# Kernel optimization log

Hardware: AMD Instinct MI355X
Metric: run time of the kernel (lower is better)

Reference implementation:

```python
import jax, jax.numpy as jnp
import numpy as np

N, E = 131072, 64
REL_SIZES = {0: (262144, 1), 1: (524288, 2), 2: (393216, 3)}  # idx_len, arity


def _mish(x):
    return x * jnp.tanh(jax.nn.softplus(x))


def _mlp(x, rw, rb, ow, ob):
    # torch MLP: output(input + mish(residual(input)))
    return (x + _mish(x @ rw + rb)) @ ow + ob


def setup_inputs() -> dict:
    key = jax.random.key(0)
    ks = jax.random.split(key, 16)

    def lin(k, fi, fo):
        k1, k2 = jax.random.split(k)
        lim = 1.0 / np.sqrt(fi)
        w = jax.random.uniform(k1, (fi, fo), jnp.float32, -lim, lim)
        b = jax.random.uniform(k2, (fo,), jnp.float32, -lim, lim)
        return w, b

    inp = {"obj_emb": jax.random.normal(ks[0], (N, E), jnp.float32)}
    for r in range(3):
        L, _ = REL_SIZES[r]
        inp[f"rel{r}_idx"] = jax.random.randint(ks[1 + r], (L,), 0, N, jnp.int64)
    for r in range(3):
        _, a = REL_SIZES[r]
        d = a * E
        w, b = lin(ks[4 + 2 * r], d, d)
        inp[f"r{r}_res_w"], inp[f"r{r}_res_b"] = w, b
        w, b = lin(ks[5 + 2 * r], d, d)
        inp[f"r{r}_out_w"], inp[f"r{r}_out_b"] = w, b
    w, b = lin(ks[10], 2 * E, 2 * E)
    inp["upd_res_w"], inp["upd_res_b"] = w, b
    w, b = lin(ks[11], 2 * E, E)
    inp["upd_out_w"], inp["upd_out_b"] = w, b
    return inp


def _forward(obj_emb, idxs, rel_params, upd_params):
    n, e = obj_emb.shape
    outs = []
    for (idx, a), (rw, rb, ow, ob) in zip(idxs, rel_params):
        g = obj_emb[idx].reshape(-1, a * e)          # gather -> [T, a*E]
        outs.append((idx, _mlp(g, rw, rb, ow, ob).reshape(-1, e)))
    # First scatter_reduce_('amax', include_self=False): positions written by
    # relation 0 ignore the initial 0; all other positions keep/compete with 0.
    written0 = jnp.zeros((n,), bool).at[idxs[0][0]].set(True)
    m = jnp.broadcast_to(jnp.where(written0[:, None], -jnp.inf, 0.0).astype(obj_emb.dtype), (n, e))
    for idx, out in outs:
        m = m.at[idx].max(out)
    m = jax.lax.stop_gradient(m)
    s = jnp.full((n, e), 1e-16, obj_emb.dtype)
    for idx, out in outs:
        s = s.at[idx].add(jnp.exp(12.0 * (out - m[idx])))
    max_msg = jnp.log(s) / 12.0 + m
    return _mlp(jnp.concatenate([max_msg, obj_emb], axis=1), *upd_params)


def reference(obj_emb, rel0_idx, rel1_idx, rel2_idx,
              r0_res_w, r0_res_b, r0_out_w, r0_out_b,
              r1_res_w, r1_res_b, r1_out_w, r1_out_b,
              r2_res_w, r2_res_b, r2_out_w, r2_out_b,
              upd_res_w, upd_res_b, upd_out_w, upd_out_b):
    idxs = [(rel0_idx, 1), (rel1_idx, 2), (rel2_idx, 3)]
    rel_params = [
        (r0_res_w, r0_res_b, r0_out_w, r0_out_b),
        (r1_res_w, r1_res_b, r1_out_w, r1_out_b),
        (r2_res_w, r2_res_b, r2_out_w, r2_out_b),
    ]
    return _forward(obj_emb, idxs, rel_params,
                    (upd_res_w, upd_res_b, upd_out_w, upd_out_b))
```

## Files before the change

### kernel.cpp

```cpp
#include <hip/hip_runtime.h>
#include <stdint.h>

typedef unsigned short u16;
typedef __bf16 bf16x8 __attribute__((ext_vector_type(8)));
typedef float floatx4 __attribute__((ext_vector_type(4)));

#define N_OBJ    131072
#define L0R      262144
#define L1R      524288
#define L2R      393216
#define TOTI     (L0R + L1R + L2R)


__device__ __forceinline__ float bf2f(u16 u) {
  union { uint32_t i; float f; } v; v.i = ((uint32_t)u) << 16; return v.f;
}
__device__ __forceinline__ u16 f2bf(float f) {
  union { float f; uint32_t i; } v; v.f = f;
  uint32_t r = (v.i + 0x7FFFu + ((v.i >> 16) & 1u)) >> 16;
  return (u16)r;
}
__device__ __forceinline__ uint4 pack8(const float* sp) {
  float4 f0 = *(const float4*)(sp);
  float4 f1 = *(const float4*)(sp + 4);
  uint4 v;
  v.x = (uint32_t)f2bf(f0.x) | ((uint32_t)f2bf(f0.y) << 16);
  v.y = (uint32_t)f2bf(f0.z) | ((uint32_t)f2bf(f0.w) << 16);
  v.z = (uint32_t)f2bf(f1.x) | ((uint32_t)f2bf(f1.y) << 16);
  v.w = (uint32_t)f2bf(f1.z) | ((uint32_t)f2bf(f1.w) << 16);
  return v;
}
__device__ __forceinline__ float mish_f(float x) {
  float t = __expf(fminf(x, 30.f));
  float u = 1.f + t; u = u * u;
  return x * (u - 1.f) / (u + 1.f);
}

__global__ __launch_bounds__(256) void ebf_kernel(
    const float* __restrict__ src, u16* __restrict__ dst)
{
  size_t g = (size_t)blockIdx.x * 256 + threadIdx.x;
  *(uint4*)(dst + g * 8) = pack8(src + g * 8);
}

__global__ __launch_bounds__(256) void norm_kernel(
    const int* __restrict__ r0, const int* __restrict__ r1,
    const int* __restrict__ r2, int* __restrict__ n, int* __restrict__ cnt,
    unsigned char* __restrict__ flag)
{
  int g = blockIdx.x * 256 + (int)threadIdx.x;
  const int* src; int off;
  if (g < L0R)              { src = r0; off = g; }
  else if (g < L0R + L1R)   { src = r1; off = g - L0R; }
  else                      { src = r2; off = g - L0R - L1R; }
  int lane = (int)threadIdx.x & 63;
  int probe = src[2 * lane + 1];
  bool i64 = (__ballot(probe == 0) == ~0ull);
  int v = i64 ? src[2 * off] : src[off];
  n[g] = v;
  if (g < L0R) flag[v] = 1;
  if (cnt) atomicAdd(&cnt[v], 1);
}

__global__ __launch_bounds__(256) void prep_kernel(
    const float* w0, const float* w1, const float* w2, const float* w3,
    const float* w4, const float* w5, const float* w6, const float* w7,
    u16* __restrict__ wt)
{
  int b = blockIdx.x;
  const float* srcs[8] = {w0, w1, w2, w3, w4, w5, w6, w7};
  const int fi[8]   = {64, 64, 128, 128, 192, 192, 128, 128};
  const int fo[8]   = {64, 64, 128, 128, 192, 192, 128, 64};
  const int boff[9] = {0, 16, 32, 96, 160, 304, 448, 512, 544};
  const int woff[8] = {0, 4096, 8192, 24576, 40960, 77824, 114688, 131072};
  int m = 0;
  #pragma unroll
  for (int j = 0; j < 8; ++j) if (b >= boff[j + 1]) m = j + 1;
  int e = (b - boff[m]) * 256 + (int)threadIdx.x;
  int k = e / fo[m];
  int n = e - k * fo[m];
  wt[woff[m] + n * fi[m] + k] = f2bf(srcs[m][e]);
}

__global__ __launch_bounds__(256) void scan_a(
    const int* __restrict__ count, int* __restrict__ thrpre,
    int* __restrict__ blocksum)
{
  int tid = (int)threadIdx.x, b = blockIdx.x;
  int o = b * 1024 + tid * 4;
  int t = count[o] + count[o + 1] + count[o + 2] + count[o + 3];
  __shared__ int sd[256];
  sd[tid] = t; __syncthreads();
  for (int off = 1; off < 256; off <<= 1) {
    int v = (tid >= off) ? sd[tid - off] : 0;
    __syncthreads();
    sd[tid] += v;
    __syncthreads();
  }
  thrpre[b * 256 + tid] = sd[tid] - t;
  if (tid == 255) blocksum[b] = sd[tid];
}
__global__ __launch_bounds__(128) void scan_b(int* __restrict__ blocksum)
{
  int tid = (int)threadIdx.x;
  int t = blocksum[tid];
  __shared__ int sd[128];
  sd[tid] = t; __syncthreads();
  for (int off = 1; off < 128; off <<= 1) {
    int v = (tid >= off) ? sd[tid - off] : 0;
    __syncthreads();
    sd[tid] += v;
    __syncthreads();
  }
  blocksum[tid] = sd[tid] - t;
}
__global__ __launch_bounds__(256) void scan_c(
    const int* __restrict__ count, const int* __restrict__ thrpre,
    const int* __restrict__ blocksum, int* __restrict__ offsets,
    int* __restrict__ cursor)
{
  int tid = (int)threadIdx.x, b = blockIdx.x;
  int o = b * 1024 + tid * 4;
  int base = blocksum[b] + thrpre[b * 256 + tid];
  #pragma unroll
  for (int j = 0; j < 4; ++j) {
    offsets[o + j] = base;
    cursor[o + j] = base;
    base += count[o + j];
  }
}

template<int D, int DOUT, int EBF>
__device__ __forceinline__ void mlp_body(
    char* smem, const float* __restrict__ srcF, const u16* __restrict__ srcB,
    const int* __restrict__ idx, int bidx,
    const u16* __restrict__ rwt, const float* __restrict__ rb,
    const u16* __restrict__ owt, const float* __restrict__ ob,
    u16* __restrict__ msg, int* __restrict__ cursor)
{
  constexpr int A = D / 64;
  constexpr int PITCH = D + 8;
  constexpr int KI = D / 32;
  constexpr int CT1 = D / 64;
  constexpr int CT2 = DOUT / 64;
  u16*   g_lds  = (u16*)smem;
  float* b1_lds = (float*)(smem + 64 * PITCH * 2);
  float* b2_lds = b1_lds + D;
  int*   i_lds  = (int*)(b2_lds + DOUT);
  int*   p_lds  = i_lds + 64 * A;

  const int tid = threadIdx.x;
  const int wave = tid >> 6;
  const int lane = tid & 63;
  const int q = lane >> 4;
  const int i = lane & 15;
  const int t0 = bidx * 64;

  for (int c = tid; c < D; c += 256) b1_lds[c] = rb[c];
  for (int c = tid; c < DOUT; c += 256) b2_lds[c] = ob[c];
  for (int c = tid; c < 64 * A; c += 256) {
    int obj = idx[t0 * A + c];
    i_lds[c] = obj;
    p_lds[c] = atomicAdd(&cursor[obj], 1);
  }

  for (int c = tid; c < 64 * A * 8; c += 256) {
    int e = c >> 3, p = c & 7;
    int r = e / A, sl = e - r * A;
    int obj = idx[(t0 + r) * A + sl];
    uint4 val = EBF ? *(const uint4*)(srcB + (size_t)obj * 64 + p * 8)
                    : pack8(srcF + (size_t)obj * 64 + p * 8);
    *(uint4*)(&g_lds[r * PITCH + sl * 64 + p * 8]) = val;
  }
  __syncthreads();

  bf16x8 af[KI];

  bf16x8 b1[CT1][KI];
  #pragma unroll
  for (int j = 0; j < CT1; ++j)
    #pragma unroll
    for (int k = 0; k < KI; ++k)
      b1[j][k] = *(const bf16x8*)(rwt +
          (size_t)((wave * CT1 + j) * 16 + i) * D + k * 32 + q * 8);

  floatx4 acc1[4][CT1];
  #pragma unroll
  for (int rt = 0; rt < 4; ++rt)
    #pragma unroll
    for (int j = 0; j < CT1; ++j) acc1[rt][j] = (floatx4)0.f;

  #pragma unroll
  for (int rt = 0; rt < 4; ++rt) {
    #pragma unroll
    for (int k = 0; k < KI; ++k)
      af[k] = *(const bf16x8*)(&g_lds[(rt * 16 + i) * PITCH + k * 32 + q * 8]);
    #pragma unroll
    for (int j = 0; j < CT1; ++j)
      #pragma unroll
      for (int k = 0; k < KI; ++k)
        acc1[rt][j] = __builtin_amdgcn_mfma_f32_16x16x32_bf16(
            af[k], b1[j][k], acc1[rt][j], 0, 0, 0);
  }
  __syncthreads();

  #pragma unroll
  for (int rt = 0; rt < 4; ++rt)
    #pragma unroll
    for (int j = 0; j < CT1; ++j) {
      int col = (wave * CT1 + j) * 16 + i;
      #pragma unroll
      for (int r = 0; r < 4; ++r) {
        int row = rt * 16 + q * 4 + r;
        float h = acc1[rt][j][r] + b1_lds[col];
        float g = bf2f(g_lds[row * PITCH + col]);
        g_lds[row * PITCH + col] = f2bf(g + mish_f(h));
      }
    }
  __syncthreads();

  bf16x8 b2[CT2][KI];
  #pragma unroll
  for (int j = 0; j < CT2; ++j)
    #pragma unroll
    for (int k = 0; k < KI; ++k)
      b2[j][k] = *(const bf16x8*)(owt +
          (size_t)((wave * CT2 + j) * 16 + i) * D + k * 32 + q * 8);

  floatx4 acc2[4][CT2];
  #pragma unroll
  for (int rt = 0; rt < 4; ++rt)
    #pragma unroll
    for (int j = 0; j < CT2; ++j) acc2[rt][j] = (floatx4)0.f;

  #pragma unroll
  for (int rt = 0; rt < 4; ++rt) {
    #pragma unroll
    for (int k = 0; k < KI; ++k)
      af[k] = *(const bf16x8*)(&g_lds[(rt * 16 + i) * PITCH + k * 32 + q * 8]);
    #pragma unroll
    for (int j = 0; j < CT2; ++j)
      #pragma unroll
      for (int k = 0; k < KI; ++k)
        acc2[rt][j] = __builtin_amdgcn_mfma_f32_16x16x32_bf16(
            af[k], b2[j][k], acc2[rt][j], 0, 0, 0);
  }

  #pragma unroll
  for (int rt = 0; rt < 4; ++rt)
    #pragma unroll
    for (int j = 0; j < CT2; ++j) {
      int col = (wave * CT2 + j) * 16 + i;
      int slot = col >> 6, cc = col & 63;
      #pragma unroll
      for (int r = 0; r < 4; ++r) {
        int row = rt * 16 + q * 4 + r;
        float y = acc2[rt][j][r] + b2_lds[col];
        int pos = p_lds[row * A + slot];
        msg[(size_t)pos * 64 + cc] = f2bf(__expf(fminf(12.f * y, 82.f)));
      }
    }
}

template<int EBF>
__global__ __launch_bounds__(256, 3) void rel_merged(
    const float* __restrict__ srcF, const u16* __restrict__ ebf,
    const int* __restrict__ nidx, const u16* __restrict__ wt,
    const float* __restrict__ r0rb, const float* __restrict__ r0ob,
    const float* __restrict__ r1rb, const float* __restrict__ r1ob,
    const float* __restrict__ r2rb, const float* __restrict__ r2ob,
    u16* __restrict__ msg, int* __restrict__ cursor)
{
  extern __shared__ char smem[];
  int b = blockIdx.x;
  if (b < 4096)
    mlp_body<64, 64, EBF>(smem, srcF, ebf, nidx, b,
                          wt + 0, r0rb, wt + 4096, r0ob, msg, cursor);
  else if (b < 8192)
    mlp_body<128, 128, EBF>(smem, srcF, ebf, nidx + L0R, b - 4096,
                            wt + 8192, r1rb, wt + 24576, r1ob, msg, cursor);
  else
    mlp_body<192, 192, EBF>(smem, srcF, ebf, nidx + L0R + L1R, b - 8192,
                            wt + 40960, r2rb, wt + 77824, r2ob, msg, cursor);
}

template<int EBF>
__global__ __launch_bounds__(256, 4) void upd_fused(
    const float* __restrict__ srcF, const u16* __restrict__ ebf,
    const u16* __restrict__ msg, const int* __restrict__ count,
    const int* __restrict__ offsets, const unsigned char* __restrict__ flag,
    const u16* __restrict__ rwt, const float* __restrict__ rb,
    const u16* __restrict__ owt, const float* __restrict__ ob,
    float* __restrict__ dstF)
{
  constexpr int D = 128, DOUT = 64;
  constexpr int PITCH = D + 8;
  constexpr int KI = D / 32;
  constexpr int CT1 = 2, CT2 = 1;
  __shared__ alignas(16) u16 g_lds[64 * PITCH];
  __shared__ float b1_lds[D];
  __shared__ float b2_lds[DOUT];

  const int tid = threadIdx.x;
  const int wave = tid >> 6;
  const int lane = tid & 63;
  const int q = lane >> 4;
  const int i = lane & 15;
  const int t0 = blockIdx.x * 64;

  for (int c = tid; c < D; c += 256) b1_lds[c] = rb[c];
  for (int c = tid; c < DOUT; c += 256) b2_lds[c] = ob[c];

  for (int c = tid; c < 64 * 2 * 8; c += 256) {
    int e = c >> 3, p = c & 7;
    int r = e >> 1, sl = e & 1;
    int o = t0 + r;
    if (sl == 0) {
      int deg = count[o], st = offsets[o];
      const u16* bp = msg + (size_t)st * 64 + p * 8;
      float s[8] = {0.f, 0.f, 0.f, 0.f, 0.f, 0.f, 0.f, 0.f};
      for (int j = 0; j < deg; ++j) {
        union { uint4 v; u16 a[8]; } ld;
        ld.v = *(const uint4*)(bp + (size_t)j * 64);
        #pragma unroll
        for (int k = 0; k < 8; ++k) s[k] += bf2f(ld.a[k]);
      }
      float add = flag[o] ? 1e-37f : 1e-16f;
      u16 tmp[8];
      #pragma unroll
      for (int k = 0; k < 8; ++k)
        tmp[k] = f2bf(__logf(s[k] + add) * (1.f / 12.f));
      *(uint4*)(&g_lds[r * PITCH + p * 8]) = *(uint4*)tmp;
    } else {
      uint4 val = EBF ? *(const uint4*)(ebf + (size_t)o * 64 + p * 8)
                      : pack8(srcF + (size_t)o * 64 + p * 8);
      *(uint4*)(&g_lds[r * PITCH + 64 + p * 8]) = val;
    }
  }
  __syncthreads();

  bf16x8 af[KI];

  bf16x8 b1[CT1][KI];
  #pragma unroll
  for (int j = 0; j < CT1; ++j)
    #pragma unroll
    for (int k = 0; k < KI; ++k)
      b1[j][k] = *(const bf16x8*)(rwt +
          (size_t)((wave * CT1 + j) * 16 + i) * D + k * 32 + q * 8);

  floatx4 acc1[4][CT1];
  #pragma unroll
  for (int rt = 0; rt < 4; ++rt)
    #pragma unroll
    for (int j = 0; j < CT1; ++j) acc1[rt][j] = (floatx4)0.f;

  #pragma unroll
  for (int rt = 0; rt < 4; ++rt) {
    #pragma unroll
    for (int k = 0; k < KI; ++k)
      af[k] = *(const bf16x8*)(&g_lds[(rt * 16 + i) * PITCH + k * 32 + q * 8]);
    #pragma unroll
    for (int j = 0; j < CT1; ++j)
      #pragma unroll
      for (int k = 0; k < KI; ++k)
        acc1[rt][j] = __builtin_amdgcn_mfma_f32_16x16x32_bf16(
            af[k], b1[j][k], acc1[rt][j], 0, 0, 0);
  }
  __syncthreads();

  #pragma unroll
  for (int rt = 0; rt < 4; ++rt)
    #pragma unroll
    for (int j = 0; j < CT1; ++j) {
      int col = (wave * CT1 + j) * 16 + i;
      #pragma unroll
      for (int r = 0; r < 4; ++r) {
        int row = rt * 16 + q * 4 + r;
        float h = acc1[rt][j][r] + b1_lds[col];
        float g = bf2f(g_lds[row * PITCH + col]);
        g_lds[row * PITCH + col] = f2bf(g + mish_f(h));
      }
    }
  __syncthreads();

  bf16x8 b2[CT2][KI];
  #pragma unroll
  for (int j = 0; j < CT2; ++j)
    #pragma unroll
    for (int k = 0; k < KI; ++k)
      b2[j][k] = *(const bf16x8*)(owt +
          (size_t)((wave * CT2 + j) * 16 + i) * D + k * 32 + q * 8);

  floatx4 acc2[4][CT2];
  #pragma unroll
  for (int rt = 0; rt < 4; ++rt)
    #pragma unroll
    for (int j = 0; j < CT2; ++j) acc2[rt][j] = (floatx4)0.f;

  #pragma unroll
  for (int rt = 0; rt < 4; ++rt) {
    #pragma unroll
    for (int k = 0; k < KI; ++k)
      af[k] = *(const bf16x8*)(&g_lds[(rt * 16 + i) * PITCH + k * 32 + q * 8]);
    #pragma unroll
    for (int j = 0; j < CT2; ++j)
      #pragma unroll
      for (int k = 0; k < KI; ++k)
        acc2[rt][j] = __builtin_amdgcn_mfma_f32_16x16x32_bf16(
            af[k], b2[j][k], acc2[rt][j], 0, 0, 0);
  }

  #pragma unroll
  for (int rt = 0; rt < 4; ++rt) {
    int col = wave * 16 + i;
    #pragma unroll
    for (int r = 0; r < 4; ++r) {
      int row = rt * 16 + q * 4 + r;
      dstF[(size_t)(t0 + row) * 64 + col] = acc2[0][0][r * 0 + 0] * 0.f
          + acc2[rt][0][r] + b2_lds[col];
    }
  }
}

template<int D, int DOUT, int MODE>
__global__ __launch_bounds__(256, (D >= 192) ? 3 : 4) void mlp_fb(
    const float* __restrict__ srcF, const u16* __restrict__ srcM,
    const int* __restrict__ idx,
    const u16* __restrict__ rwt, const float* __restrict__ rb,
    const u16* __restrict__ owt, const float* __restrict__ ob,
    float* __restrict__ dstF, float* __restrict__ sAt)
{
  constexpr int A = D / 64;
  constexpr int PITCH = D + 8;
  constexpr int KI = D / 32;
  constexpr int CT1 = D / 64;
  constexpr int CT2 = DOUT / 64;
  __shared__ alignas(16) u16 g_lds[64 * PITCH];
  __shared__ float b1_lds[D];
  __shared__ float b2_lds[DOUT];
  __shared__ int i_lds[64 * A];

  const int tid = threadIdx.x;
  const int wave = tid >> 6;
  const int lane = tid & 63;
  const int q = lane >> 4;
  const int i = lane & 15;
  const int t0 = blockIdx.x * 64;

  for (int c = tid; c < D; c += 256) b1_lds[c] = rb[c];
  for (int c = tid; c < DOUT; c += 256) b2_lds[c] = ob[c];
  if (MODE != 1)
    for (int c = tid; c < 64 * A; c += 256) i_lds[c] = idx[t0 * A + c];

  for (int c = tid; c < 64 * A * 8; c += 256) {
    int e = c >> 3, p = c & 7;
    int r = e / A, sl = e - r * A;
    uint4 val;
    if (MODE != 1) {
      int obj = idx[(t0 + r) * A + sl];
      val = pack8(srcF + (size_t)obj * 64 + p * 8);
    } else {
      if (sl == 0) val = *(const uint4*)(srcM + (size_t)(t0 + r) * 64 + p * 8);
      else         val = pack8(srcF + (size_t)(t0 + r) * 64 + p * 8);
    }
    *(uint4*)(&g_lds[r * PITCH + sl * 64 + p * 8]) = val;
  }
  __syncthreads();

  bf16x8 af[KI];
  bf16x8 b1[CT1][KI];
  #pragma unroll
  for (int j = 0; j < CT1; ++j)
    #pragma unroll
    for (int k = 0; k < KI; ++k)
      b1[j][k] = *(const bf16x8*)(rwt +
          (size_t)((wave * CT1 + j) * 16 + i) * D + k * 32 + q * 8);
  floatx4 acc1[4][CT1];
  #pragma unroll
  for (int rt = 0; rt < 4; ++rt)
    #pragma unroll
    for (int j = 0; j < CT1; ++j) acc1[rt][j] = (floatx4)0.f;
  #pragma unroll
  for (int rt = 0; rt < 4; ++rt) {
    #pragma unroll
    for (int k = 0; k < KI; ++k)
      af[k] = *(const bf16x8*)(&g_lds[(rt * 16 + i) * PITCH + k * 32 + q * 8]);
    #pragma unroll
    for (int j = 0; j < CT1; ++j)
      #pragma unroll
      for (int k = 0; k < KI; ++k)
        acc1[rt][j] = __builtin_amdgcn_mfma_f32_16x16x32_bf16(
            af[k], b1[j][k], acc1[rt][j], 0, 0, 0);
  }
  __syncthreads();
  #pragma unroll
  for (int rt = 0; rt < 4; ++rt)
    #pragma unroll
    for (int j = 0; j < CT1; ++j) {
      int col = (wave * CT1 + j) * 16 + i;
      #pragma unroll
      for (int r = 0; r < 4; ++r) {
        int row = rt * 16 + q * 4 + r;
        float h = acc1[rt][j][r] + b1_lds[col];
        float g = bf2f(g_lds[row * PITCH + col]);
        g_lds[row * PITCH + col] = f2bf(g + mish_f(h));
      }
    }
  __syncthreads();
  bf16x8 b2[CT2][KI];
  #pragma unroll
  for (int j = 0; j < CT2; ++j)
    #pragma unroll
    for (int k = 0; k < KI; ++k)
      b2[j][k] = *(const bf16x8*)(owt +
          (size_t)((wave * CT2 + j) * 16 + i) * D + k * 32 + q * 8);
  floatx4 acc2[4][CT2];
  #pragma unroll
  for (int rt = 0; rt < 4; ++rt)
    #pragma unroll
    for (int j = 0; j < CT2; ++j) acc2[rt][j] = (floatx4)0.f;
  #pragma unroll
  for (int rt = 0; rt < 4; ++rt) {
    #pragma unroll
    for (int k = 0; k < KI; ++k)
      af[k] = *(const bf16x8*)(&g_lds[(rt * 16 + i) * PITCH + k * 32 + q * 8]);
    #pragma unroll
    for (int j = 0; j < CT2; ++j)
      #pragma unroll
      for (int k = 0; k < KI; ++k)
        acc2[rt][j] = __builtin_amdgcn_mfma_f32_16x16x32_bf16(
            af[k], b2[j][k], acc2[rt][j], 0, 0, 0);
  }
  #pragma unroll
  for (int rt = 0; rt < 4; ++rt)
    #pragma unroll
    for (int j = 0; j < CT2; ++j) {
      int col = (wave * CT2 + j) * 16 + i;
      #pragma unroll
      for (int r = 0; r < 4; ++r) {
        int row = rt * 16 + q * 4 + r;
        float y = acc2[rt][j][r] + b2_lds[col];
        if (MODE == 2) {
          int slot = col >> 6, cc = col & 63;
          int obj = i_lds[row * A + slot];
          atomicAdd(&sAt[(size_t)obj * 64 + cc], __expf(fminf(12.f * y, 82.f)));
        } else {
          dstF[(size_t)(t0 + row) * 64 + col] = y;
        }
      }
    }
}

__global__ __launch_bounds__(256) void final_kernel(
    const float* __restrict__ s, const unsigned char* __restrict__ flag,
    u16* __restrict__ maxmsg)
{
  int tid = (int)threadIdx.x;
  int o = blockIdx.x * 64 + (tid >> 2);
  int c0 = (tid & 3) * 16;
  float add = flag[o] ? 1e-37f : 1e-16f;
  const float* sp = s + (size_t)o * 64 + c0;
  u16* mp = maxmsg + (size_t)o * 64 + c0;
  u16 tmp[16];
  #pragma unroll
  for (int j = 0; j < 16; ++j)
    tmp[j] = f2bf(__logf(sp[j] + add) * (1.f / 12.f));
  *(uint4*)(mp)     = *(uint4*)(tmp);
  *(uint4*)(mp + 8) = *(uint4*)(tmp + 8);
}

extern "C" void kernel_launch(void* const* d_in, const int* in_sizes, int n_in,
                              void* d_out, int out_size, void* d_ws, size_t ws_size,
                              hipStream_t stream)
{
  (void)in_sizes; (void)n_in; (void)out_size;
  const float* obj_emb = (const float*)d_in[0];
  const float* r0rb = (const float*)d_in[5];
  const float* r0ob = (const float*)d_in[7];
  const float* r1rb = (const float*)d_in[9];
  const float* r1ob = (const float*)d_in[11];
  const float* r2rb = (const float*)d_in[13];
  const float* r2ob = (const float*)d_in[15];
  const float* urb  = (const float*)d_in[17];
  const float* uob  = (const float*)d_in[19];
  float* out = (float*)d_out;
  char* ws = (char*)d_ws;

  const size_t NEED1 = 174605312ull;
  const size_t NEED2 = NEED1 + 16777216ull;

  if (ws_size >= NEED1) {
    u16* msg           = (u16*)(ws);
    u16* wt            = (u16*)(ws + 150994944ull);
    unsigned char* flg = (unsigned char*)(ws + 151273472ull);
    int* nidx          = (int*)(ws + 168181760ull);
    int* count         = (int*)(ws + 172900352ull);
    int* offsets       = (int*)(ws + 173424640ull);
    int* cursor        = (int*)(ws + 173948928ull);
    int* thrpre        = (int*)(ws + 174473216ull);
    int* blocksum      = (int*)(ws + 174604288ull);
    u16* ebf           = (u16*)(ws + 174605312ull);
    bool use_ebf = ws_size >= NEED2;

    hipMemsetAsync(count, 0, N_OBJ * 4, stream);
    hipMemsetAsync(flg, 0, N_OBJ, stream);

    if (use_ebf) ebf_kernel<<<4096, 256, 0, stream>>>(obj_emb, ebf);
    norm_kernel<<<TOTI / 256, 256, 0, stream>>>(
        (const int*)d_in[1], (const int*)d_in[2], (const int*)d_in[3],
        nidx, count, flg);
    prep_kernel<<<544, 256, 0, stream>>>(
        (const float*)d_in[4], (const float*)d_in[6], (const float*)d_in[8],
        (const float*)d_in[10], (const float*)d_in[12], (const float*)d_in[14],
        (const float*)d_in[16], (const float*)d_in[18], wt);
    scan_a<<<128, 256, 0, stream>>>(count, thrpre, blocksum);
    scan_b<<<1, 128, 0, stream>>>(blocksum);
    scan_c<<<128, 256, 0, stream>>>(count, thrpre, blocksum, offsets, cursor);

    if (use_ebf) {
      rel_merged<1><<<10240, 256, 28672, stream>>>(
          obj_emb, ebf, nidx, wt, r0rb, r0ob, r1rb, r1ob, r2rb, r2ob, msg, cursor);
      upd_fused<1><<<2048, 256, 0, stream>>>(
          obj_emb, ebf, msg, count, offsets, flg,
          wt + 114688, urb, wt + 131072, uob, out);
    } else {
      rel_merged<0><<<10240, 256, 28672, stream>>>(
          obj_emb, ebf, nidx, wt, r0rb, r0ob, r1rb, r1ob, r2rb, r2ob, msg, cursor);
      upd_fused<0><<<2048, 256, 0, stream>>>(
          obj_emb, ebf, msg, count, offsets, flg,
          wt + 114688, urb, wt + 131072, uob, out);
    }
  } else {
    float* s           = (float*)(ws);
    u16* wt            = (u16*)(ws + 33554432ull);
    unsigned char* flg = (unsigned char*)(ws + 33832960ull);
    u16* maxmsg        = (u16*)(ws + 33964032ull);
    int* nidx          = (int*)(ws + 50741248ull);

    hipMemsetAsync(s, 0, 64ull * N_OBJ * 4ull, stream);
    hipMemsetAsync(flg, 0, N_OBJ, stream);

    norm_kernel<<<TOTI / 256, 256, 0, stream>>>(
        (const int*)d_in[1], (const int*)d_in[2], (const int*)d_in[3],
        nidx, nullptr, flg);
    prep_kernel<<<544, 256, 0, stream>>>(
        (const float*)d_in[4], (const float*)d_in[6], (const float*)d_in[8],
        (const float*)d_in[10], (const float*)d_in[12], (const float*)d_in[14],
        (const float*)d_in[16], (const float*)d_in[18], wt);

    mlp_fb<64, 64, 2><<<4096, 256, 0, stream>>>(
        obj_emb, nullptr, nidx, wt + 0, r0rb, wt + 4096, r0ob, nullptr, s);
    mlp_fb<128, 128, 2><<<4096, 256, 0, stream>>>(
        obj_emb, nullptr, nidx + L0R, wt + 8192, r1rb, wt + 24576, r1ob, nullptr, s);
    mlp_fb<192, 192, 2><<<2048, 256, 0, stream>>>(
        obj_emb, nullptr, nidx + L0R + L1R, wt + 40960, r2rb, wt + 77824, r2ob,
        nullptr, s);

    final_kernel<<<N_OBJ / 64, 256, 0, stream>>>(s, flg, maxmsg);

    mlp_fb<128, 64, 1><<<2048, 256, 0, stream>>>(
        obj_emb, maxmsg, nullptr, wt + 114688, urb, wt + 131072, uob, out, nullptr);
  }
}
```

Measured before the change: 399.9 us.

## Merge preprocessing kernels, stage message writes through LDS, interleave relation blocks

```diff
diff --git a/kernel.cpp b/kernel.cpp
--- a/kernel.cpp
+++ b/kernel.cpp
@@ -19,6 +19,9 @@
   union { float f; uint32_t i; } v; v.f = f;
   uint32_t r = (v.i + 0x7FFFu + ((v.i >> 16) & 1u)) >> 16;
   return (u16)r;
+}
+__device__ __forceinline__ u16 f2bf_t(float f) {
+  return (u16)(__float_as_uint(f) >> 16);
 }
 __device__ __forceinline__ uint4 pack8(const float* sp) {
   float4 f0 = *(const float4*)(sp);
@@ -33,53 +36,52 @@
 __device__ __forceinline__ float mish_f(float x) {
   float t = __expf(fminf(x, 30.f));
   float u = 1.f + t; u = u * u;
-  return x * (u - 1.f) / (u + 1.f);
-}
-
-__global__ __launch_bounds__(256) void ebf_kernel(
-    const float* __restrict__ src, u16* __restrict__ dst)
-{
-  size_t g = (size_t)blockIdx.x * 256 + threadIdx.x;
-  *(uint4*)(dst + g * 8) = pack8(src + g * 8);
-}
-
-__global__ __launch_bounds__(256) void norm_kernel(
+  return x * (u - 1.f) * __builtin_amdgcn_rcpf(u + 1.f);
+}
+#define C12 17.312340490667560f
+
+__global__ __launch_bounds__(256) void pre_kernel(
+    const float* __restrict__ emb, u16* __restrict__ ebf,
     const int* __restrict__ r0, const int* __restrict__ r1,
-    const int* __restrict__ r2, int* __restrict__ n, int* __restrict__ cnt,
-    unsigned char* __restrict__ flag)
-{
-  int g = blockIdx.x * 256 + (int)threadIdx.x;
-  const int* src; int off;
-  if (g < L0R)              { src = r0; off = g; }
-  else if (g < L0R + L1R)   { src = r1; off = g - L0R; }
-  else                      { src = r2; off = g - L0R - L1R; }
-  int lane = (int)threadIdx.x & 63;
-  int probe = src[2 * lane + 1];
-  bool i64 = (__ballot(probe == 0) == ~0ull);
-  int v = i64 ? src[2 * off] : src[off];
-  n[g] = v;
-  if (g < L0R) flag[v] = 1;
-  if (cnt) atomicAdd(&cnt[v], 1);
-}
-
-__global__ __launch_bounds__(256) void prep_kernel(
+    const int* __restrict__ r2, int* __restrict__ nidx,
+    int* __restrict__ cnt, unsigned char* __restrict__ flag,
     const float* w0, const float* w1, const float* w2, const float* w3,
     const float* w4, const float* w5, const float* w6, const float* w7,
-    u16* __restrict__ wt)
+    u16* __restrict__ wt, int use_ebf)
 {
   int b = blockIdx.x;
-  const float* srcs[8] = {w0, w1, w2, w3, w4, w5, w6, w7};
-  const int fi[8]   = {64, 64, 128, 128, 192, 192, 128, 128};
-  const int fo[8]   = {64, 64, 128, 128, 192, 192, 128, 64};
-  const int boff[9] = {0, 16, 32, 96, 160, 304, 448, 512, 544};
-  const int woff[8] = {0, 4096, 8192, 24576, 40960, 77824, 114688, 131072};
-  int m = 0;
-  #pragma unroll
-  for (int j = 0; j < 8; ++j) if (b >= boff[j + 1]) m = j + 1;
-  int e = (b - boff[m]) * 256 + (int)threadIdx.x;
-  int k = e / fo[m];
-  int n = e - k * fo[m];
-  wt[woff[m] + n * fi[m] + k] = f2bf(srcs[m][e]);
+  if (b < 4096) {
+    if (!use_ebf) return;
+    size_t g = (size_t)b * 256 + threadIdx.x;
+    *(uint4*)(ebf + g * 8) = pack8(emb + g * 8);
+  } else if (b < 4096 + TOTI / 256) {
+    int g = (b - 4096) * 256 + (int)threadIdx.x;
+    const int* src; int off;
+    if (g < L0R)            { src = r0; off = g; }
+    else if (g < L0R + L1R) { src = r1; off = g - L0R; }
+    else                    { src = r2; off = g - L0R - L1R; }
+    int lane = (int)threadIdx.x & 63;
+    int probe = src[2 * lane + 1];
+    bool i64 = (__ballot(probe == 0) == ~0ull);
+    int v = i64 ? src[2 * off] : src[off];
+    nidx[g] = v;
+    if (g < L0R) flag[v] = 1;
+    atomicAdd(&cnt[v], 1);
+  } else {
+    int bb = b - 4096 - TOTI / 256;
+    const float* srcs[8] = {w0, w1, w2, w3, w4, w5, w6, w7};
+    const int fi[8]   = {64, 64, 128, 128, 192, 192, 128, 128};
+    const int fo[8]   = {64, 64, 128, 128, 192, 192, 128, 64};
+    const int boff[9] = {0, 16, 32, 96, 160, 304, 448, 512, 544};
+    const int woff[8] = {0, 4096, 8192, 24576, 40960, 77824, 114688, 131072};
+    int m = 0;
+    #pragma unroll
+    for (int j = 0; j < 8; ++j) if (bb >= boff[j + 1]) m = j + 1;
+    int e = (bb - boff[m]) * 256 + (int)threadIdx.x;
+    int k = e / fo[m];
+    int n = e - k * fo[m];
+    wt[woff[m] + n * fi[m] + k] = f2bf(srcs[m][e]);
+  }
 }
 
 __global__ __launch_bounds__(256) void scan_a(
@@ -157,7 +159,7 @@
   const int t0 = bidx * 64;
 
   for (int c = tid; c < D; c += 256) b1_lds[c] = rb[c];
-  for (int c = tid; c < DOUT; c += 256) b2_lds[c] = ob[c];
+  for (int c = tid; c < DOUT; c += 256) b2_lds[c] = ob[c] * C12;
   for (int c = tid; c < 64 * A; c += 256) {
     int obj = idx[t0 * A + c];
     i_lds[c] = obj;
@@ -214,7 +216,7 @@
         int row = rt * 16 + q * 4 + r;
         float h = acc1[rt][j][r] + b1_lds[col];
         float g = bf2f(g_lds[row * PITCH + col]);
-        g_lds[row * PITCH + col] = f2bf(g + mish_f(h));
+        g_lds[row * PITCH + col] = f2bf_t(g + mish_f(h));
       }
     }
   __syncthreads();
@@ -245,21 +247,28 @@
         acc2[rt][j] = __builtin_amdgcn_mfma_f32_16x16x32_bf16(
             af[k], b2[j][k], acc2[rt][j], 0, 0, 0);
   }
+  __syncthreads();
 
   #pragma unroll
   for (int rt = 0; rt < 4; ++rt)
     #pragma unroll
     for (int j = 0; j < CT2; ++j) {
       int col = (wave * CT2 + j) * 16 + i;
-      int slot = col >> 6, cc = col & 63;
       #pragma unroll
       for (int r = 0; r < 4; ++r) {
         int row = rt * 16 + q * 4 + r;
-        float y = acc2[rt][j][r] + b2_lds[col];
-        int pos = p_lds[row * A + slot];
-        msg[(size_t)pos * 64 + cc] = f2bf(__expf(fminf(12.f * y, 82.f)));
+        float z = fminf(fmaf(acc2[rt][j][r], C12, b2_lds[col]), 118.f);
+        g_lds[row * PITCH + col] = f2bf_t(exp2f(z));
       }
     }
+  __syncthreads();
+  for (int c = tid; c < 64 * A * 8; c += 256) {
+    int e = c >> 3, p = c & 7;
+    int r = e / A, sl = e - r * A;
+    int pos = p_lds[r * A + sl];
+    *(uint4*)(msg + (size_t)pos * 64 + p * 8) =
+        *(const uint4*)(&g_lds[r * PITCH + sl * 64 + p * 8]);
+  }
 }
 
 template<int EBF>
@@ -273,14 +282,15 @@
 {
   extern __shared__ char smem[];
   int b = blockIdx.x;
-  if (b < 4096)
-    mlp_body<64, 64, EBF>(smem, srcF, ebf, nidx, b,
+  int g5 = b / 5, m = b - g5 * 5;
+  if (m < 2)
+    mlp_body<64, 64, EBF>(smem, srcF, ebf, nidx, g5 * 2 + m,
                           wt + 0, r0rb, wt + 4096, r0ob, msg, cursor);
-  else if (b < 8192)
-    mlp_body<128, 128, EBF>(smem, srcF, ebf, nidx + L0R, b - 4096,
+  else if (m < 4)
+    mlp_body<128, 128, EBF>(smem, srcF, ebf, nidx + L0R, g5 * 2 + (m - 2),
                             wt + 8192, r1rb, wt + 24576, r1ob, msg, cursor);
   else
-    mlp_body<192, 192, EBF>(smem, srcF, ebf, nidx + L0R + L1R, b - 8192,
+    mlp_body<192, 192, EBF>(smem, srcF, ebf, nidx + L0R + L1R, g5,
                             wt + 40960, r2rb, wt + 77824, r2ob, msg, cursor);
 }
 
@@ -340,7 +350,6 @@
   __syncthreads();
 
   bf16x8 af[KI];
-
   bf16x8 b1[CT1][KI];
   #pragma unroll
   for (int j = 0; j < CT1; ++j)
@@ -379,7 +388,7 @@
         int row = rt * 16 + q * 4 + r;
         float h = acc1[rt][j][r] + b1_lds[col];
         float g = bf2f(g_lds[row * PITCH + col]);
-        g_lds[row * PITCH + col] = f2bf(g + mish_f(h));
+        g_lds[row * PITCH + col] = f2bf_t(g + mish_f(h));
       }
     }
   __syncthreads();
@@ -417,8 +426,7 @@
     #pragma unroll
     for (int r = 0; r < 4; ++r) {
       int row = rt * 16 + q * 4 + r;
-      dstF[(size_t)(t0 + row) * 64 + col] = acc2[0][0][r * 0 + 0] * 0.f
-          + acc2[rt][0][r] + b2_lds[col];
+      dstF[(size_t)(t0 + row) * 64 + col] = acc2[rt][0][r] + b2_lds[col];
     }
   }
 }
@@ -550,6 +558,44 @@
         }
       }
     }
+}
+
+__global__ __launch_bounds__(256) void norm_fb(
+    const int* __restrict__ r0, const int* __restrict__ r1,
+    const int* __restrict__ r2, int* __restrict__ n,
+    unsigned char* __restrict__ flag)
+{
+  int g = blockIdx.x * 256 + (int)threadIdx.x;
+  const int* src; int off;
+  if (g < L0R)            { src = r0; off = g; }
+  else if (g < L0R + L1R) { src = r1; off = g - L0R; }
+  else                    { src = r2; off = g - L0R - L1R; }
+  int lane = (int)threadIdx.x & 63;
+  int probe = src[2 * lane + 1];
+  bool i64 = (__ballot(probe == 0) == ~0ull);
+  int v = i64 ? src[2 * off] : src[off];
+  n[g] = v;
+  if (g < L0R) flag[v] = 1;
+}
+
+__global__ __launch_bounds__(256) void prep_fb(
+    const float* w0, const float* w1, const float* w2, const float* w3,
+    const float* w4, const float* w5, const float* w6, const float* w7,
+    u16* __restrict__ wt)
+{
+  int b = blockIdx.x;
+  const float* srcs[8] = {w0, w1, w2, w3, w4, w5, w6, w7};
+  const int fi[8]   = {64, 64, 128, 128, 192, 192, 128, 128};
+  const int fo[8]   = {64, 64, 128, 128, 192, 192, 128, 64};
+  const int boff[9] = {0, 16, 32, 96, 160, 304, 448, 512, 544};
+  const int woff[8] = {0, 4096, 8192, 24576, 40960, 77824, 114688, 131072};
+  int m = 0;
+  #pragma unroll
+  for (int j = 0; j < 8; ++j) if (b >= boff[j + 1]) m = j + 1;
+  int e = (b - boff[m]) * 256 + (int)threadIdx.x;
+  int k = e / fo[m];
+  int n = e - k * fo[m];
+  wt[woff[m] + n * fi[m] + k] = f2bf(srcs[m][e]);
 }
 
 __global__ __launch_bounds__(256) void final_kernel(
@@ -601,19 +647,18 @@
     int* thrpre        = (int*)(ws + 174473216ull);
     int* blocksum      = (int*)(ws + 174604288ull);
     u16* ebf           = (u16*)(ws + 174605312ull);
-    bool use_ebf = ws_size >= NEED2;
+    int use_ebf = (ws_size >= NEED2) ? 1 : 0;
 
     hipMemsetAsync(count, 0, N_OBJ * 4, stream);
     hipMemsetAsync(flg, 0, N_OBJ, stream);
 
-    if (use_ebf) ebf_kernel<<<4096, 256, 0, stream>>>(obj_emb, ebf);
-    norm_kernel<<<TOTI / 256, 256, 0, stream>>>(
+    pre_kernel<<<4096 + TOTI / 256 + 544, 256, 0, stream>>>(
+        obj_emb, ebf,
         (const int*)d_in[1], (const int*)d_in[2], (const int*)d_in[3],
-        nidx, count, flg);
-    prep_kernel<<<544, 256, 0, stream>>>(
+        nidx, count, flg,
         (const float*)d_in[4], (const float*)d_in[6], (const float*)d_in[8],
         (const float*)d_in[10], (const float*)d_in[12], (const float*)d_in[14],
-        (const float*)d_in[16], (const float*)d_in[18], wt);
+        (const float*)d_in[16], (const float*)d_in[18], wt, use_ebf);
     scan_a<<<128, 256, 0, stream>>>(count, thrpre, blocksum);
     scan_b<<<1, 128, 0, stream>>>(blocksum);
     scan_c<<<128, 256, 0, stream>>>(count, thrpre, blocksum, offsets, cursor);
@@ -641,10 +686,9 @@
     hipMemsetAsync(s, 0, 64ull * N_OBJ * 4ull, stream);
     hipMemsetAsync(flg, 0, N_OBJ, stream);
 
-    norm_kernel<<<TOTI / 256, 256, 0, stream>>>(
-        (const int*)d_in[1], (const int*)d_in[2], (const int*)d_in[3],
-        nidx, nullptr, flg);
-    prep_kernel<<<544, 256, 0, stream>>>(
+    norm_fb<<<TOTI / 256, 256, 0, stream>>>(
+        (const int*)d_in[1], (const int*)d_in[2], (const int*)d_in[3], nidx, flg);
+    prep_fb<<<544, 256, 0, stream>>>(
         (const float*)d_in[4], (const float*)d_in[6], (const float*)d_in[8],
         (const float*)d_in[10], (const float*)d_in[12], (const float*)d_in[14],
         (const float*)d_in[16], (const float*)d_in[18], wt);
```

Result: faster. 387.3 us (-3.2%).
